# Kernel optimization log

Measured on AMD Instinct MI355X. Metric: run time of the kernel, lower is better.

## Reference

```python
import jax, jax.numpy as jnp
import numpy as np
import math

M = 0.2
S = 30.0
COS_M = math.cos(M); SIN_M = math.sin(M)
TH = math.cos(math.pi - M)          # threshold used in torch.where
MM = math.sin(math.pi - M) * M      # linear penalty past threshold
EPS_LS = 0.1                        # CrossEntropyLoss label_smoothing


def _normalize(a, axis=-1):
    return a / jnp.clip(jnp.linalg.norm(a, axis=axis, keepdims=True), 1e-12)


def setup_inputs() -> dict:
    key = jax.random.key(0)
    k1, k2, k3, k4, k5 = jax.random.split(key, 5)
    B, D, C = 2048, 512, 10000
    x = jax.random.normal(k1, (B, D), dtype=jnp.float32)
    label = jax.random.randint(k2, (B,), 0, 1000)  # valid class ids, ~2 per class
    std = math.sqrt(2.0 / (C + D))  # xavier_normal gain=1
    weight = jax.random.normal(k3, (C, D), dtype=jnp.float32) * std    # self.weight (w)
    weight_m = jax.random.normal(k4, (C, D), dtype=jnp.float32) * std  # self.weight_m (wq)
    weight_n = jax.random.uniform(k5, (C, D), dtype=jnp.float32)       # self.weight_n (wk)
    return {"x": x, "label": label, "weight": weight, "weight_m": weight_m, "weight_n": weight_n}


def reference(x, label, weight, weight_m, weight_n):
    B = x.shape[0]
    C = weight.shape[0]
    xn = _normalize(x)                                   # [B, D]

    # ---- AAM (ArcFace) branch ----
    cosine = xn @ _normalize(weight).T                   # [B, C]
    sine = jnp.sqrt(jnp.clip(1.0 - cosine * cosine, 0.0, 1.0))
    phi = cosine * COS_M - sine * SIN_M
    phi = jnp.where(cosine - TH > 0, phi, cosine - MM)
    one_hot = jax.nn.one_hot(label, C, dtype=cosine.dtype)
    output = (one_hot * phi + (1.0 - one_hot) * cosine) * S
    logp = jax.nn.log_softmax(output, axis=-1)
    q_target = one_hot * (1.0 - EPS_LS) + EPS_LS / C     # label smoothing
    aam_loss = -jnp.mean(jnp.sum(q_target * logp, axis=-1))

    # ---- Control-Contrastive branch ----
    label_matrix = label[:, None] == label[None, :]      # [B, B] bool
    q = xn @ _normalize(weight_m[label]).T               # [B, B]
    k = xn @ _normalize(weight_n[label]).T               # [B, B]
    sim = q * k                                          # elementwise, [B, B]

    lm = label_matrix.astype(sim.dtype)
    ap_m = jnp.sum(sim * lm, axis=1) / jnp.sum(lm, axis=1)  # masked row means, [B]
    ap = jnp.diagonal(sim)                                   # [B]
    an = jnp.where(label_matrix, 0.0, sim)                   # [B, B]

    cos_ap = jnp.clip(ap, 0.0, 1.0)
    sin_ap = jnp.sqrt(jnp.clip(1.0 - cos_ap, 0.0, 1.0))
    cos_apm = jnp.clip(ap_m, 0.0, 1.0)
    sin_apm = jnp.sqrt(jnp.clip(1.0 - cos_apm, 0.0, 1.0))
    cos_an = jnp.clip(an, 0.0, 1.0)
    sin_an = jnp.sqrt(jnp.clip(1.0 - cos_an, 0.0, 1.0))

    phi_pm_c = cos_ap * cos_apm - sin_ap * sin_apm       # [B]
    phi_pm_s = jnp.sqrt(jnp.clip(1.0 - phi_pm_c, 0.0, 1.0))
    phi_pm = phi_pm_c * COS_M - phi_pm_s * SIN_M
    logit_neg = 1.0 - phi_pm                              # [B]

    # torch broadcasting [B,B]*[B] -> broadcast over rows (axis 0)
    phi_nm_s = sin_an * cos_apm[None, :] + cos_an * sin_apm[None, :]
    phi_nm_c = jnp.sqrt(jnp.clip(1.0 - phi_nm_s, 0.0, 1.0))
    phi_nm = phi_nm_s * COS_M - phi_nm_c * SIN_M          # [B, B]

    # ragged boolean-indexed logsumexp == masked logsumexp over whole matrix
    lse_n = jax.nn.logsumexp(jnp.where(label_matrix, -jnp.inf, phi_nm))
    lse_neg = jax.nn.logsumexp(logit_neg)
    cc_loss = jax.nn.softplus(lse_n + lse_neg)

    return aam_loss + cc_loss
```

## Files before the change

kernel.cpp:

```cpp
#include <hip/hip_runtime.h>
#include <hip/hip_bf16.h>

typedef unsigned short u16;
typedef unsigned char u8;
typedef unsigned int u32;
typedef _Float16 f16;
typedef _Float16 f16x8 __attribute__((ext_vector_type(8)));
typedef float f32x4 __attribute__((ext_vector_type(4)));
typedef unsigned int u32x4 __attribute__((ext_vector_type(4)));
typedef unsigned int u32x2 __attribute__((ext_vector_type(2)));
typedef long v2i64 __attribute__((ext_vector_type(2)));

constexpr int BATCH = 2048;
constexpr int DIM   = 512;
constexpr int NCLS  = 10000;
constexpr int NPAD  = 10240;

#define F_S     30.0f
#define F_COS_M 0.9800665778412416f
#define F_SIN_M 0.19866933079506122f
#define F_TH   (-0.9800665778412416f)
#define F_MM    0.03973386615901224f

#define G_AAM  1280
#define G_CC    512

static __device__ __forceinline__ float clampf(float v, float lo, float hi) {
    return fminf(fmaxf(v, lo), hi);
}
static __device__ __forceinline__ u32 pk4_fp8(float a, float b, float c, float d) {
    u32 w = __builtin_amdgcn_cvt_pk_fp8_f32(a, b, 0, false);
    w = __builtin_amdgcn_cvt_pk_fp8_f32(c, d, w, true);
    return w;
}
static __device__ __forceinline__ void glds16(const void* g, void* l) {
    __builtin_amdgcn_global_load_lds(
        (const __attribute__((address_space(1))) unsigned int*)g,
        (__attribute__((address_space(3))) unsigned int*)l, 16, 0, 0);
}
static __device__ __forceinline__ float blk_sum(float v, float* sh, int t) {
#pragma unroll
    for (int o = 32; o > 0; o >>= 1) v += __shfl_down(v, o, 64);
    __syncthreads();
    if ((t & 63) == 0) sh[t >> 6] = v;
    __syncthreads();
    return sh[0] + sh[1] + sh[2] + sh[3];
}

__global__ __launch_bounds__(256) void norm_all_kernel(const float* __restrict__ x,
                                                       const float* __restrict__ w,
                                                       const float* __restrict__ wm,
                                                       const float* __restrict__ wn,
                                                       const int* __restrict__ label,
                                                       u8* __restrict__ xnb,
                                                       u8* __restrict__ wb,
                                                       u8* __restrict__ wqb,
                                                       u8* __restrict__ wkb,
                                                       float* __restrict__ zacc) {
    const int t = threadIdx.x, lane = t & 63, wv = t >> 6;
    const int b = blockIdx.x;
    if (b < 33) zacc[b * 256 + t] = 0.f;

    const int row = b * 4 + wv;
    const float* src;
    u8* dst;
    if (row < BATCH) {
        src = x + (size_t)row * DIM;
        dst = xnb + (size_t)row * DIM;
    } else if (row < BATCH + NPAD) {
        const int r = row - BATCH;
        dst = wb + (size_t)r * DIM;
        if (r >= NCLS) {
            u32x2 z = {0, 0};
            *(u32x2*)(dst + lane * 8) = z;
            return;
        }
        src = w + (size_t)r * DIM;
    } else if (row < BATCH + NPAD + BATCH) {
        const int i = row - (BATCH + NPAD);
        src = wm + (size_t)label[i] * DIM;
        dst = wqb + (size_t)i * DIM;
    } else {
        const int i = row - (BATCH + NPAD + BATCH);
        src = wn + (size_t)label[i] * DIM;
        dst = wkb + (size_t)i * DIM;
    }
    const float4 v0 = ((const float4*)src)[lane * 2];
    const float4 v1 = ((const float4*)src)[lane * 2 + 1];
    float s = v0.x * v0.x + v0.y * v0.y + v0.z * v0.z + v0.w * v0.w
            + v1.x * v1.x + v1.y * v1.y + v1.z * v1.z + v1.w * v1.w;
#pragma unroll
    for (int o = 32; o > 0; o >>= 1) s += __shfl_xor(s, o, 64);
    const float inv = 1.0f / fmaxf(sqrtf(s), 1e-12f);
    u32 lo = pk4_fp8(v0.x * inv, v0.y * inv, v0.z * inv, v0.w * inv);
    u32 hi = pk4_fp8(v1.x * inv, v1.y * inv, v1.z * inv, v1.w * inv);
    const int p = 8 * (lane >> 3) + 4 * (lane & 1) + ((lane >> 1) & 3);
    u32x2 o2;
    o2[0] = __shfl(lo, p, 64);
    o2[1] = __shfl(hi, p, 64);
    *(u32x2*)(dst + lane * 8) = o2;
}

__global__ __launch_bounds__(256) void gemm_fused_kernel(const u8* __restrict__ A,
                                                         const u8* __restrict__ Bw,
                                                         const u8* __restrict__ Bq,
                                                         const u8* __restrict__ Bk,
                                                         const int* __restrict__ label,
                                                         float* __restrict__ sumexp,
                                                         float* __restrict__ sumlogit,
                                                         float* __restrict__ philab,
                                                         f16* __restrict__ sim,
                                                         float* __restrict__ msum,
                                                         float* __restrict__ mcnt,
                                                         float* __restrict__ ap) {
    __shared__ __align__(16) u8 sA[128 * 128];
    __shared__ __align__(16) u8 sB[128 * 128];
    __shared__ float red0[128];
    __shared__ float red1[128];

    const int t = threadIdx.x;
    const int lane = t & 63, wave = t >> 6;
    const int fr = lane & 15, quad = lane >> 4;
    const int swz = fr & 7;

    if (t < 128) { red0[t] = 0.f; red1[t] = 0.f; }

    const int srow = t >> 3;
    const int sgs  = (t & 7) ^ (srow & 7);

    if (blockIdx.x < G_AAM) {
        const int flat = blockIdx.x;
        const int xcd = flat & 7, r = flat >> 3;
        const int bm = r & 15;
        const int bn = (r >> 4) * 8 + xcd;

        const int wm = (wave >> 1) * 64, wn = (wave & 1) * 64;
        const u8* ag = A  + (size_t)(bm * 128 + srow) * DIM + sgs * 16;
        const u8* bg = Bw + (size_t)(bn * 128 + srow) * DIM + sgs * 16;

        f32x4 acc[4][4] = {};

        for (int kb = 0; kb < 4; kb++) {
            const int ko = kb * 128;
#pragma unroll
            for (int s = 0; s < 4; s++) {
                glds16(ag + (size_t)(s * 32) * DIM + ko, &sA[s * 4096 + t * 16]);
                glds16(bg + (size_t)(s * 32) * DIM + ko, &sB[s * 4096 + t * 16]);
            }
            __syncthreads();
#pragma unroll
            for (int blkr = 0; blkr < 2; blkr++) {
                const int slot = ((blkr << 2) | quad) ^ swz;
                v2i64 a8[4], b8[4];
#pragma unroll
                for (int f = 0; f < 4; f++) {
                    a8[f] = __builtin_bit_cast(v2i64, *(const u32x4*)&sA[(wm + f * 16 + fr) * 128 + slot * 16]);
                    b8[f] = __builtin_bit_cast(v2i64, *(const u32x4*)&sB[(wn + f * 16 + fr) * 128 + slot * 16]);
                }
#pragma unroll
                for (int i = 0; i < 4; i++)
#pragma unroll
                    for (int j = 0; j < 4; j++) {
                        acc[i][j] = __builtin_amdgcn_mfma_f32_16x16x32_fp8_fp8(a8[i][0], b8[j][0], acc[i][j], 0, 0, 0);
                        acc[i][j] = __builtin_amdgcn_mfma_f32_16x16x32_fp8_fp8(a8[i][1], b8[j][1], acc[i][j], 0, 0, 0);
                    }
            }
            __syncthreads();
        }

#pragma unroll
        for (int i = 0; i < 4; i++) {
#pragma unroll
            for (int r3 = 0; r3 < 4; r3++) {
                const int ml = wm + i * 16 + quad * 4 + r3;
                const int mg = bm * 128 + ml;
                const int lab = label[mg];
                float esum = 0.f, lsum = 0.f;
#pragma unroll
                for (int j = 0; j < 4; j++) {
                    const int ng = bn * 128 + wn + j * 16 + fr;
                    if (ng < NCLS) {
                        float cv = acc[i][j][r3];
                        float logit;
                        if (ng == lab) {
                            float sine = sqrtf(clampf(1.f - cv * cv, 0.f, 1.f));
                            float phi = cv * F_COS_M - sine * F_SIN_M;
                            float val = ((cv - F_TH) > 0.f) ? phi : (cv - F_MM);
                            logit = F_S * val;
                            philab[mg] = logit;
                        } else {
                            logit = F_S * cv;
                        }
                        esum += __expf(logit);
                        lsum += logit;
                    }
                }
#pragma unroll
                for (int off = 1; off < 16; off <<= 1) {
                    esum += __shfl_xor(esum, off, 64);
                    lsum += __shfl_xor(lsum, off, 64);
                }
                if (fr == 0) {
                    atomicAdd(&red0[ml], esum);
                    atomicAdd(&red1[ml], lsum);
                }
            }
        }
        __syncthreads();
        if (t < 128) {
            atomicAdd(&sumexp[bm * 128 + t], red0[t]);
            atomicAdd(&sumlogit[bm * 128 + t], red1[t]);
        }
    } else {
        const int c = blockIdx.x - G_AAM;
        const int xcd = c & 7, r = c >> 3;
        const int bm = r & 15;
        const int bn = (r >> 4) * 8 + xcd;

        const int wm = (wave >> 1) * 64, wn = (wave & 1) * 32;
        u8* Qs = sB;
        u8* Ks = sB + 8192;

        const u8* ag = A  + (size_t)(bm * 128 + srow) * DIM + sgs * 16;
        const u8* qg = Bq + (size_t)(bn * 64 + srow) * DIM + sgs * 16;
        const u8* kg = Bk + (size_t)(bn * 64 + srow) * DIM + sgs * 16;

        f32x4 aq[4][2] = {};
        f32x4 ak[4][2] = {};

        for (int kb = 0; kb < 4; kb++) {
            const int ko = kb * 128;
#pragma unroll
            for (int s = 0; s < 4; s++)
                glds16(ag + (size_t)(s * 32) * DIM + ko, &sA[s * 4096 + t * 16]);
#pragma unroll
            for (int s = 0; s < 2; s++) {
                glds16(qg + (size_t)(s * 32) * DIM + ko, &Qs[s * 4096 + t * 16]);
                glds16(kg + (size_t)(s * 32) * DIM + ko, &Ks[s * 4096 + t * 16]);
            }
            __syncthreads();
#pragma unroll
            for (int blkr = 0; blkr < 2; blkr++) {
                const int slot = ((blkr << 2) | quad) ^ swz;
                v2i64 a8[4], q8[2], k8[2];
#pragma unroll
                for (int f = 0; f < 4; f++)
                    a8[f] = __builtin_bit_cast(v2i64, *(const u32x4*)&sA[(wm + f * 16 + fr) * 128 + slot * 16]);
#pragma unroll
                for (int f = 0; f < 2; f++) {
                    q8[f] = __builtin_bit_cast(v2i64, *(const u32x4*)&Qs[(wn + f * 16 + fr) * 128 + slot * 16]);
                    k8[f] = __builtin_bit_cast(v2i64, *(const u32x4*)&Ks[(wn + f * 16 + fr) * 128 + slot * 16]);
                }
#pragma unroll
                for (int i = 0; i < 4; i++)
#pragma unroll
                    for (int j = 0; j < 2; j++) {
                        aq[i][j] = __builtin_amdgcn_mfma_f32_16x16x32_fp8_fp8(a8[i][0], q8[j][0], aq[i][j], 0, 0, 0);
                        aq[i][j] = __builtin_amdgcn_mfma_f32_16x16x32_fp8_fp8(a8[i][1], q8[j][1], aq[i][j], 0, 0, 0);
                        ak[i][j] = __builtin_amdgcn_mfma_f32_16x16x32_fp8_fp8(a8[i][0], k8[j][0], ak[i][j], 0, 0, 0);
                        ak[i][j] = __builtin_amdgcn_mfma_f32_16x16x32_fp8_fp8(a8[i][1], k8[j][1], ak[i][j], 0, 0, 0);
                    }
            }
            __syncthreads();
        }

        int lab_n[2];
#pragma unroll
        for (int j = 0; j < 2; j++) lab_n[j] = label[bn * 64 + wn + j * 16 + fr];

#pragma unroll
        for (int i = 0; i < 4; i++) {
#pragma unroll
            for (int r3 = 0; r3 < 4; r3++) {
                const int ml = wm + i * 16 + quad * 4 + r3;
                const int mg = bm * 128 + ml;
                const int lm = label[mg];
                float ms = 0.f, mc = 0.f;
#pragma unroll
                for (int j = 0; j < 2; j++) {
                    const int ng = bn * 64 + wn + j * 16 + fr;
                    float s = aq[i][j][r3] * ak[i][j][r3];
                    sim[(size_t)mg * BATCH + ng] = (f16)s;
                    if (lab_n[j] == lm) { ms += s; mc += 1.f; }
                    if (mg == ng) ap[mg] = s;
                }
#pragma unroll
                for (int off = 1; off < 16; off <<= 1) {
                    ms += __shfl_xor(ms, off, 64);
                    mc += __shfl_xor(mc, off, 64);
                }
                if (fr == 0) {
                    atomicAdd(&red0[ml], ms);
                    atomicAdd(&red1[ml], mc);
                }
            }
        }
        __syncthreads();
        if (t < 128) {
            atomicAdd(&msum[bm * 128 + t], red0[t]);
            atomicAdd(&mcnt[bm * 128 + t], red1[t]);
        }
    }
}

__global__ __launch_bounds__(256) void cc_pass2_kernel(const f16* __restrict__ sim,
                                                       const int* __restrict__ label,
                                                       const float* __restrict__ msum,
                                                       const float* __restrict__ mcnt,
                                                       const float* __restrict__ ap,
                                                       const float* __restrict__ sumexp,
                                                       const float* __restrict__ sumlogit,
                                                       const float* __restrict__ philab,
                                                       float* __restrict__ zn,
                                                       float* __restrict__ zneg,
                                                       float* __restrict__ accA,
                                                       unsigned* __restrict__ tick,
                                                       float* __restrict__ out) {
    __shared__ __align__(16) float cam_s[BATCH];
    __shared__ __align__(16) float sam_s[BATCH];
    __shared__ float sh[4];
    const int t = threadIdx.x, b = blockIdx.x;

    for (int j = t; j < BATCH; j += 256) {
        float cam = clampf(msum[j] / mcnt[j], 0.f, 1.f);
        cam_s[j] = cam;
        sam_s[j] = sqrtf(clampf(1.f - cam, 0.f, 1.f));
    }
    __syncthreads();

    float acc = 0.f;
#pragma unroll
    for (int row = 0; row < 4; row++) {
        const int i = b * 4 + row;
        const int li = label[i];
        const f16x8 v = ((const f16x8*)(sim + (size_t)i * BATCH))[t];
        const int4 l0 = ((const int4*)label)[t * 2];
        const int4 l1 = ((const int4*)label)[t * 2 + 1];
        const f32x4 ca0 = ((const f32x4*)cam_s)[t * 2];
        const f32x4 ca1 = ((const f32x4*)cam_s)[t * 2 + 1];
        const f32x4 sa0 = ((const f32x4*)sam_s)[t * 2];
        const f32x4 sa1 = ((const f32x4*)sam_s)[t * 2 + 1];
#pragma unroll
        for (int e = 0; e < 8; e++) {
            const int lj = (e < 4) ? ((const int*)&l0)[e] : ((const int*)&l1)[e - 4];
            if (lj != li) {
                float can = clampf((float)v[e], 0.f, 1.f);
                float caj = (e < 4) ? ca0[e] : ca1[e - 4];
                float saj = (e < 4) ? sa0[e] : sa1[e - 4];
                float san = sqrtf(clampf(1.f - can, 0.f, 1.f));
                float pns = san * caj + can * saj;
                float pnc = sqrtf(clampf(1.f - pns, 0.f, 1.f));
                acc += __expf(pns * F_COS_M - pnc * F_SIN_M);
            }
        }
    }
    acc = blk_sum(acc, sh, t);

    if (t == 0) {
        float apart = 0.f, epart = 0.f;
#pragma unroll
        for (int row = 0; row < 4; row++) {
            const int rr = b * 4 + row;
            float lse = logf(sumexp[rr]);
            apart += 0.9f * (philab[rr] - lse) + 1e-5f * (sumlogit[rr] - (float)NCLS * lse);
            float cam = cam_s[rr], sam = sam_s[rr];
            float cap = clampf(ap[rr], 0.f, 1.f);
            float sap = sqrtf(clampf(1.f - cap, 0.f, 1.f));
            float ppc = cap * cam - sap * sam;
            float pps = sqrtf(clampf(1.f - ppc, 0.f, 1.f));
            epart += __expf(1.f - (ppc * F_COS_M - pps * F_SIN_M));
        }
        atomicAdd(zn, acc);
        atomicAdd(accA, apart);
        atomicAdd(zneg, epart);
        unsigned old = __hip_atomic_fetch_add(tick, 1u, __ATOMIC_ACQ_REL, __HIP_MEMORY_SCOPE_AGENT);
        if (old == 511u) {
            float znv = __hip_atomic_load(zn,   __ATOMIC_RELAXED, __HIP_MEMORY_SCOPE_AGENT);
            float aav = __hip_atomic_load(accA, __ATOMIC_RELAXED, __HIP_MEMORY_SCOPE_AGENT);
            float zgv = __hip_atomic_load(zneg, __ATOMIC_RELAXED, __HIP_MEMORY_SCOPE_AGENT);
            float aam = -aav / (float)BATCH;
            float z = logf(znv) + logf(zgv);
            float cc = (z > 0.f) ? (z + log1pf(__expf(-z))) : log1pf(__expf(z));
            out[0] = aam + cc;
        }
    }
}

extern "C" void kernel_launch(void* const* d_in, const int* in_sizes, int n_in,
                              void* d_out, int out_size, void* d_ws, size_t ws_size,
                              hipStream_t stream) {
    const float* x        = (const float*)d_in[0];
    const int*   label    = (const int*)d_in[1];
    const float* weight   = (const float*)d_in[2];
    const float* weight_m = (const float*)d_in[3];
    const float* weight_n = (const float*)d_in[4];
    float* out = (float*)d_out;
    char* ws = (char*)d_ws;

    const size_t o_xnb  = 0;
    const size_t o_wb   = o_xnb + (size_t)BATCH * DIM;
    const size_t o_wqb  = o_wb  + (size_t)NPAD * DIM;
    const size_t o_wkb  = o_wqb + (size_t)BATCH * DIM;
    const size_t o_sim  = o_wkb + (size_t)BATCH * DIM;
    const size_t o_misc = o_sim + (size_t)BATCH * BATCH * 2;

    u8* xnb = (u8*)(ws + o_xnb);
    u8* wb  = (u8*)(ws + o_wb);
    u8* wqb = (u8*)(ws + o_wqb);
    u8* wkb = (u8*)(ws + o_wkb);
    f16* sim = (f16*)(ws + o_sim);
    float* mf  = (float*)(ws + o_misc);

    float* sumexp   = mf;
    float* sumlogit = mf + 2048;
    float* msum     = mf + 4096;
    float* mcnt     = mf + 6144;
    float* zn       = mf + 8192;
    float* zneg     = mf + 8193;
    float* accA     = mf + 8194;
    unsigned* tick  = (unsigned*)(mf + 8195);
    float* philab  = mf + 8448;
    float* ap      = mf + 10496;

    norm_all_kernel<<<(BATCH + NPAD + 2 * BATCH) / 4, 256, 0, stream>>>(
        x, weight, weight_m, weight_n, label, xnb, wb, wqb, wkb, mf);

    gemm_fused_kernel<<<G_AAM + G_CC, 256, 0, stream>>>(
        xnb, wb, wqb, wkb, label,
        sumexp, sumlogit, philab, sim, msum, mcnt, ap);

    cc_pass2_kernel<<<512, 256, 0, stream>>>(
        sim, label, msum, mcnt, ap,
        sumexp, sumlogit, philab, zn, zneg, accA, tick, out);
}
```

Measured before the change: 184.0 us.

## Double-buffer fused GEMM K-loop with async global-to-LDS prefetch

The fused fp8 GEMM main loop is restructured from four 128-wide K steps with synchronous staging into eight 64-wide K steps over two ping-pong LDS buffers. The next K slice is prefetched while MFMAs run on the current one, using explicit vmcnt waits, raw barriers and raised wave priority around the MFMA block. LDS footprint stays at 32KB, with a new swizzle for the 64-byte rows, and launch bounds now request 4 blocks per CU. The goal is to hide global load latency behind compute. The cost is more barriers per tile and a risk of register pressure from the occupancy hint.

```diff
diff --git a/kernel.cpp b/kernel.cpp
--- a/kernel.cpp
+++ b/kernel.cpp
@@ -101,32 +101,32 @@
     *(u32x2*)(dst + lane * 8) = o2;
 }
 
-__global__ __launch_bounds__(256) void gemm_fused_kernel(const u8* __restrict__ A,
-                                                         const u8* __restrict__ Bw,
-                                                         const u8* __restrict__ Bq,
-                                                         const u8* __restrict__ Bk,
-                                                         const int* __restrict__ label,
-                                                         float* __restrict__ sumexp,
-                                                         float* __restrict__ sumlogit,
-                                                         float* __restrict__ philab,
-                                                         f16* __restrict__ sim,
-                                                         float* __restrict__ msum,
-                                                         float* __restrict__ mcnt,
-                                                         float* __restrict__ ap) {
-    __shared__ __align__(16) u8 sA[128 * 128];
-    __shared__ __align__(16) u8 sB[128 * 128];
+__global__ __launch_bounds__(256, 4) void gemm_fused_kernel(const u8* __restrict__ A,
+                                                            const u8* __restrict__ Bw,
+                                                            const u8* __restrict__ Bq,
+                                                            const u8* __restrict__ Bk,
+                                                            const int* __restrict__ label,
+                                                            float* __restrict__ sumexp,
+                                                            float* __restrict__ sumlogit,
+                                                            float* __restrict__ philab,
+                                                            f16* __restrict__ sim,
+                                                            float* __restrict__ msum,
+                                                            float* __restrict__ mcnt,
+                                                            float* __restrict__ ap) {
+    __shared__ __align__(16) u8 sA[2][8192];
+    __shared__ __align__(16) u8 sB[2][8192];
     __shared__ float red0[128];
     __shared__ float red1[128];
 
     const int t = threadIdx.x;
     const int lane = t & 63, wave = t >> 6;
     const int fr = lane & 15, quad = lane >> 4;
-    const int swz = fr & 7;
+    const int gl = quad ^ ((fr >> 1) & 3);
 
     if (t < 128) { red0[t] = 0.f; red1[t] = 0.f; }
 
-    const int srow = t >> 3;
-    const int sgs  = (t & 7) ^ (srow & 7);
+    const int srow = t >> 2;
+    const int sg   = (t & 3) ^ ((t >> 3) & 3);
 
     if (blockIdx.x < G_AAM) {
         const int flat = blockIdx.x;
@@ -135,38 +135,54 @@
         const int bn = (r >> 4) * 8 + xcd;
 
         const int wm = (wave >> 1) * 64, wn = (wave & 1) * 64;
-        const u8* ag = A  + (size_t)(bm * 128 + srow) * DIM + sgs * 16;
-        const u8* bg = Bw + (size_t)(bn * 128 + srow) * DIM + sgs * 16;
+        const u8* ag = A  + (size_t)(bm * 128 + srow) * DIM + sg * 16;
+        const u8* bg = Bw + (size_t)(bn * 128 + srow) * DIM + sg * 16;
 
         f32x4 acc[4][4] = {};
 
-        for (int kb = 0; kb < 4; kb++) {
-            const int ko = kb * 128;
-#pragma unroll
-            for (int s = 0; s < 4; s++) {
-                glds16(ag + (size_t)(s * 32) * DIM + ko, &sA[s * 4096 + t * 16]);
-                glds16(bg + (size_t)(s * 32) * DIM + ko, &sB[s * 4096 + t * 16]);
-            }
-            __syncthreads();
-#pragma unroll
-            for (int blkr = 0; blkr < 2; blkr++) {
-                const int slot = ((blkr << 2) | quad) ^ swz;
-                v2i64 a8[4], b8[4];
-#pragma unroll
-                for (int f = 0; f < 4; f++) {
-                    a8[f] = __builtin_bit_cast(v2i64, *(const u32x4*)&sA[(wm + f * 16 + fr) * 128 + slot * 16]);
-                    b8[f] = __builtin_bit_cast(v2i64, *(const u32x4*)&sB[(wn + f * 16 + fr) * 128 + slot * 16]);
-                }
-#pragma unroll
-                for (int i = 0; i < 4; i++)
-#pragma unroll
-                    for (int j = 0; j < 4; j++) {
-                        acc[i][j] = __builtin_amdgcn_mfma_f32_16x16x32_fp8_fp8(a8[i][0], b8[j][0], acc[i][j], 0, 0, 0);
-                        acc[i][j] = __builtin_amdgcn_mfma_f32_16x16x32_fp8_fp8(a8[i][1], b8[j][1], acc[i][j], 0, 0, 0);
-                    }
-            }
-            __syncthreads();
-        }
+#define STAGE_AAM(buf, ko)                                              \
+        do {                                                            \
+            glds16(ag + (ko),            &sA[buf][t * 16]);             \
+            glds16(ag + 64 * DIM + (ko), &sA[buf][4096 + t * 16]);      \
+            glds16(bg + (ko),            &sB[buf][t * 16]);             \
+            glds16(bg + 64 * DIM + (ko), &sB[buf][4096 + t * 16]);      \
+        } while (0)
+
+        STAGE_AAM(0, 0);
+#pragma unroll
+        for (int kb = 0; kb < 8; kb++) {
+            const int cur = kb & 1;
+            if (kb < 7) {
+                STAGE_AAM(cur ^ 1, (kb + 1) * 64);
+                asm volatile("s_waitcnt vmcnt(4)" ::: "memory");
+            } else {
+                asm volatile("s_waitcnt vmcnt(0)" ::: "memory");
+            }
+            __builtin_amdgcn_s_barrier();
+            asm volatile("" ::: "memory");
+
+            const u8* sAc = sA[cur];
+            const u8* sBc = sB[cur];
+            v2i64 a8[4], b8[4];
+#pragma unroll
+            for (int f = 0; f < 4; f++) {
+                a8[f] = __builtin_bit_cast(v2i64, *(const u32x4*)&sAc[(wm + f * 16 + fr) * 64 + gl * 16]);
+                b8[f] = __builtin_bit_cast(v2i64, *(const u32x4*)&sBc[(wn + f * 16 + fr) * 64 + gl * 16]);
+            }
+            __builtin_amdgcn_s_setprio(1);
+#pragma unroll
+            for (int i = 0; i < 4; i++)
+#pragma unroll
+                for (int j = 0; j < 4; j++) {
+                    acc[i][j] = __builtin_amdgcn_mfma_f32_16x16x32_fp8_fp8(a8[i][0], b8[j][0], acc[i][j], 0, 0, 0);
+                    acc[i][j] = __builtin_amdgcn_mfma_f32_16x16x32_fp8_fp8(a8[i][1], b8[j][1], acc[i][j], 0, 0, 0);
+                }
+            __builtin_amdgcn_s_setprio(0);
+            asm volatile("s_waitcnt lgkmcnt(0)" ::: "memory");
+            __builtin_amdgcn_s_barrier();
+            asm volatile("" ::: "memory");
+        }
+#undef STAGE_AAM
 
 #pragma unroll
         for (int i = 0; i < 4; i++) {
@@ -218,51 +234,62 @@
         const int bn = (r >> 4) * 8 + xcd;
 
         const int wm = (wave >> 1) * 64, wn = (wave & 1) * 32;
-        u8* Qs = sB;
-        u8* Ks = sB + 8192;
-
-        const u8* ag = A  + (size_t)(bm * 128 + srow) * DIM + sgs * 16;
-        const u8* qg = Bq + (size_t)(bn * 64 + srow) * DIM + sgs * 16;
-        const u8* kg = Bk + (size_t)(bn * 64 + srow) * DIM + sgs * 16;
+
+        const u8* ag = A  + (size_t)(bm * 128 + srow) * DIM + sg * 16;
+        const u8* qg = Bq + (size_t)(bn * 64 + srow) * DIM + sg * 16;
+        const u8* kg = Bk + (size_t)(bn * 64 + srow) * DIM + sg * 16;
 
         f32x4 aq[4][2] = {};
         f32x4 ak[4][2] = {};
 
-        for (int kb = 0; kb < 4; kb++) {
-            const int ko = kb * 128;
-#pragma unroll
-            for (int s = 0; s < 4; s++)
-                glds16(ag + (size_t)(s * 32) * DIM + ko, &sA[s * 4096 + t * 16]);
-#pragma unroll
-            for (int s = 0; s < 2; s++) {
-                glds16(qg + (size_t)(s * 32) * DIM + ko, &Qs[s * 4096 + t * 16]);
-                glds16(kg + (size_t)(s * 32) * DIM + ko, &Ks[s * 4096 + t * 16]);
-            }
-            __syncthreads();
-#pragma unroll
-            for (int blkr = 0; blkr < 2; blkr++) {
-                const int slot = ((blkr << 2) | quad) ^ swz;
-                v2i64 a8[4], q8[2], k8[2];
-#pragma unroll
-                for (int f = 0; f < 4; f++)
-                    a8[f] = __builtin_bit_cast(v2i64, *(const u32x4*)&sA[(wm + f * 16 + fr) * 128 + slot * 16]);
-#pragma unroll
-                for (int f = 0; f < 2; f++) {
-                    q8[f] = __builtin_bit_cast(v2i64, *(const u32x4*)&Qs[(wn + f * 16 + fr) * 128 + slot * 16]);
-                    k8[f] = __builtin_bit_cast(v2i64, *(const u32x4*)&Ks[(wn + f * 16 + fr) * 128 + slot * 16]);
-                }
-#pragma unroll
-                for (int i = 0; i < 4; i++)
-#pragma unroll
-                    for (int j = 0; j < 2; j++) {
-                        aq[i][j] = __builtin_amdgcn_mfma_f32_16x16x32_fp8_fp8(a8[i][0], q8[j][0], aq[i][j], 0, 0, 0);
-                        aq[i][j] = __builtin_amdgcn_mfma_f32_16x16x32_fp8_fp8(a8[i][1], q8[j][1], aq[i][j], 0, 0, 0);
-                        ak[i][j] = __builtin_amdgcn_mfma_f32_16x16x32_fp8_fp8(a8[i][0], k8[j][0], ak[i][j], 0, 0, 0);
-                        ak[i][j] = __builtin_amdgcn_mfma_f32_16x16x32_fp8_fp8(a8[i][1], k8[j][1], ak[i][j], 0, 0, 0);
-                    }
-            }
-            __syncthreads();
-        }
+#define STAGE_CC(buf, ko)                                               \
+        do {                                                            \
+            glds16(ag + (ko),            &sA[buf][t * 16]);             \
+            glds16(ag + 64 * DIM + (ko), &sA[buf][4096 + t * 16]);      \
+            glds16(qg + (ko),            &sB[buf][t * 16]);             \
+            glds16(kg + (ko),            &sB[buf][4096 + t * 16]);      \
+        } while (0)
+
+        STAGE_CC(0, 0);
+#pragma unroll
+        for (int kb = 0; kb < 8; kb++) {
+            const int cur = kb & 1;
+            if (kb < 7) {
+                STAGE_CC(cur ^ 1, (kb + 1) * 64);
+                asm volatile("s_waitcnt vmcnt(4)" ::: "memory");
+            } else {
+                asm volatile("s_waitcnt vmcnt(0)" ::: "memory");
+            }
+            __builtin_amdgcn_s_barrier();
+            asm volatile("" ::: "memory");
+
+            const u8* sAc = sA[cur];
+            const u8* sBc = sB[cur];
+            v2i64 a8[4], q8[2], k8[2];
+#pragma unroll
+            for (int f = 0; f < 4; f++)
+                a8[f] = __builtin_bit_cast(v2i64, *(const u32x4*)&sAc[(wm + f * 16 + fr) * 64 + gl * 16]);
+#pragma unroll
+            for (int f = 0; f < 2; f++) {
+                q8[f] = __builtin_bit_cast(v2i64, *(const u32x4*)&sBc[(wn + f * 16 + fr) * 64 + gl * 16]);
+                k8[f] = __builtin_bit_cast(v2i64, *(const u32x4*)&sBc[4096 + (wn + f * 16 + fr) * 64 + gl * 16]);
+            }
+            __builtin_amdgcn_s_setprio(1);
+#pragma unroll
+            for (int i = 0; i < 4; i++)
+#pragma unroll
+                for (int j = 0; j < 2; j++) {
+                    aq[i][j] = __builtin_amdgcn_mfma_f32_16x16x32_fp8_fp8(a8[i][0], q8[j][0], aq[i][j], 0, 0, 0);
+                    aq[i][j] = __builtin_amdgcn_mfma_f32_16x16x32_fp8_fp8(a8[i][1], q8[j][1], aq[i][j], 0, 0, 0);
+                    ak[i][j] = __builtin_amdgcn_mfma_f32_16x16x32_fp8_fp8(a8[i][0], k8[j][0], ak[i][j], 0, 0, 0);
+                    ak[i][j] = __builtin_amdgcn_mfma_f32_16x16x32_fp8_fp8(a8[i][1], k8[j][1], ak[i][j], 0, 0, 0);
+                }
+            __builtin_amdgcn_s_setprio(0);
+            asm volatile("s_waitcnt lgkmcnt(0)" ::: "memory");
+            __builtin_amdgcn_s_barrier();
+            asm volatile("" ::: "memory");
+        }
+#undef STAGE_CC
 
         int lab_n[2];
 #pragma unroll
```

Result: faster. 172.8 us (-6.1%).
